# Performance work log

Measured on AMD Instinct MI355X. Metric: run time of the kernel, lower is better.

## Reference

```python
import jax, jax.numpy as jnp
import numpy as np

NUM_HEADS = 8
NUM_GROUPS = 32
EPS = 1e-5


def setup_inputs() -> dict:
    key = jax.random.key(0)
    k1, k2, k3 = jax.random.split(key, 3)
    B, C, H, W = 2, 512, 64, 64
    x = jax.random.normal(k1, (B, C, H, W), dtype=jnp.float32)
    gn_weight = jnp.ones((C,), dtype=jnp.float32)
    gn_bias = jnp.zeros((C,), dtype=jnp.float32)
    # small init so softmax logits are well-conditioned
    w_qkv = jax.random.normal(k2, (3 * C, C), dtype=jnp.float32) * 0.02
    w_proj = jax.random.normal(k3, (C, C), dtype=jnp.float32) * 0.02
    b_proj = jnp.zeros((C,), dtype=jnp.float32)
    return {"x": x, "gn_weight": gn_weight, "gn_bias": gn_bias,
            "w_qkv": w_qkv, "w_proj": w_proj, "b_proj": b_proj}


def group_norm(x, weight, bias):
    B, C, H, W = x.shape
    xg = x.reshape(B, NUM_GROUPS, C // NUM_GROUPS, H, W)
    mean = xg.mean(axis=(2, 3, 4), keepdims=True)
    var = xg.var(axis=(2, 3, 4), keepdims=True)
    xg = (xg - mean) * jax.lax.rsqrt(var + EPS)
    x = xg.reshape(B, C, H, W)
    return x * weight[None, :, None, None] + bias[None, :, None, None]


def reference(x, gn_weight, gn_bias, w_qkv, w_proj, b_proj):
    B, C, H, W = x.shape
    nh = NUM_HEADS
    hd = C // nh
    N = H * W

    h = group_norm(x, gn_weight, gn_bias)
    # 1x1 conv == per-pixel matmul: [B,3C,H,W]
    qkv = jnp.einsum('bchw,oc->bohw', h, w_qkv)
    # (B,3,nh,hd,N) -> (3,B,nh,N,hd)
    qkv = qkv.reshape(B, 3, nh, hd, N).transpose(1, 0, 2, 4, 3)
    q, k, v = qkv[0], qkv[1], qkv[2]

    scale = hd ** -0.5
    attn = jax.nn.softmax(jnp.einsum('bhnd,bhmd->bhnm', q, k) * scale, axis=-1)
    out = jnp.einsum('bhnm,bhmd->bhnd', attn, v)  # [B,nh,N,hd]
    out = out.transpose(0, 1, 3, 2).reshape(B, C, H, W)
    out = jnp.einsum('bchw,oc->bohw', out, w_proj) + b_proj[None, :, None, None]
    return x + out
```

## Files before the change

kernel.cpp:

```cpp
#include <hip/hip_runtime.h>
#include <math.h>

#define BB 2
#define CC 512
#define NN 4096
#define NH 8
#define HD 64
#define NG 32
#define CPG 16

typedef __attribute__((ext_vector_type(8))) short short8;
typedef __attribute__((ext_vector_type(4))) float f32x4;
typedef __attribute__((ext_vector_type(16))) float f32x16;
typedef __attribute__((ext_vector_type(2))) unsigned int u32x2;

typedef __attribute__((address_space(1))) void glb_t;
typedef __attribute__((address_space(3))) void lds_t;

__device__ __forceinline__ void async16(const void* g, void* l) {
  __builtin_amdgcn_global_load_lds((const glb_t*)g, (lds_t*)l, 16, 0, 0);
}

__device__ __forceinline__ unsigned short f2bf(float f) {
  unsigned int u = __float_as_uint(f);
  u += 0x7fffu + ((u >> 16) & 1u);
  return (unsigned short)(u >> 16);
}

__device__ __forceinline__ unsigned int cvt_pk_bf16(float a, float b) {
  unsigned int r;
  asm("v_cvt_pk_bf16_f32 %0, %1, %2" : "=v"(r) : "v"(a), "v"(b));
  return r;
}

__global__ __launch_bounds__(256) void k_gnstats(const float* __restrict__ x,
                                                 float* __restrict__ stats) {
  int b = blockIdx.x >> 5, g = blockIdx.x & 31;
  const float4* p = (const float4*)(x + (size_t)(b * CC + g * CPG) * NN);
  double s = 0.0, sq = 0.0;
  for (int i = threadIdx.x; i < (CPG * NN) / 4; i += 256) {
    float4 v = p[i];
    s  += (double)v.x + (double)v.y + (double)v.z + (double)v.w;
    sq += (double)v.x * v.x + (double)v.y * v.y + (double)v.z * v.z + (double)v.w * v.w;
  }
  __shared__ double red[512];
  red[threadIdx.x] = s; red[256 + threadIdx.x] = sq;
  __syncthreads();
  for (int off = 128; off > 0; off >>= 1) {
    if (threadIdx.x < off) {
      red[threadIdx.x] += red[threadIdx.x + off];
      red[256 + threadIdx.x] += red[256 + threadIdx.x + off];
    }
    __syncthreads();
  }
  if (threadIdx.x == 0) {
    double mean = red[0] / (double)(CPG * NN);
    double var  = red[256] / (double)(CPG * NN) - mean * mean;
    stats[(b * NG + g) * 2]     = (float)mean;
    stats[(b * NG + g) * 2 + 1] = (float)(1.0 / sqrt(var + 1e-5));
  }
}

__global__ __launch_bounds__(256) void k_gnapply(const float* __restrict__ x,
                                                 const float* __restrict__ gw,
                                                 const float* __restrict__ gb,
                                                 const float* __restrict__ stats,
                                                 unsigned short* __restrict__ hT) {
  int bid = blockIdx.x;
  int b = bid >> 9;
  int c0 = ((bid >> 6) & 7) * 64;
  int n0 = (bid & 63) * 64;
  __shared__ float tile[64 * 65];
  int t = threadIdx.x;
#pragma unroll
  for (int i = 0; i < 16; ++i) {
    int e = i * 256 + t, c = e >> 6, n = e & 63;
    int cg = c0 + c, g = cg >> 4;
    float mu = stats[(b * NG + g) * 2], rs = stats[(b * NG + g) * 2 + 1];
    float v = x[(size_t)(b * CC + cg) * NN + n0 + n];
    tile[c * 65 + n] = (v - mu) * rs * gw[cg] + gb[cg];
  }
  __syncthreads();
#pragma unroll
  for (int i = 0; i < 16; ++i) {
    int e = i * 256 + t, n = e >> 6, c = e & 63;
    hT[(size_t)(b * NN + n0 + n) * CC + c0 + c] = f2bf(tile[c * 65 + n]);
  }
}

__global__ __launch_bounds__(256) void k_cvt(const float* __restrict__ src,
                                             unsigned short* __restrict__ dst) {
  int i = (blockIdx.x * 256 + threadIdx.x) * 4;
  float4 v = *(const float4*)(src + i);
  ushort4 o;
  o.x = f2bf(v.x); o.y = f2bf(v.y); o.z = f2bf(v.z); o.w = f2bf(v.w);
  *(ushort4*)(dst + i) = o;
}

__device__ __forceinline__ void gemm_mainloop(const unsigned short* __restrict__ A,
                                              const unsigned short* __restrict__ Bm,
                                              char* smem, int m0, int n0,
                                              f32x4 acc[4][4]) {
  const int t = threadIdx.x, wave = t >> 6, lane = t & 63;
  const int l15 = lane & 15, lhi = lane >> 4;
  const int wr = wave >> 1, wc = wave & 1;
  const f32x4 fz = {0.f, 0.f, 0.f, 0.f};
#pragma unroll
  for (int mi = 0; mi < 4; ++mi)
#pragma unroll
    for (int ni = 0; ni < 4; ++ni) acc[mi][ni] = fz;

  for (int kt = 0; kt < 8; ++kt) {
    __syncthreads();
#pragma unroll
    for (int issue = 0; issue < 4; ++issue) {
      int slot = issue * 256 + t;
      int row = slot >> 3, g = slot & 7;
      async16(A + (size_t)(m0 + row) * 512 + kt * 64 + g * 8,
              smem + issue * 4096 + wave * 1024);
      async16(Bm + (size_t)(n0 + row) * 512 + kt * 64 + g * 8,
              smem + 16384 + issue * 4096 + wave * 1024);
    }
    __syncthreads();
#pragma unroll
    for (int kk = 0; kk < 2; ++kk) {
      short8 a[4], bf[4];
#pragma unroll
      for (int mi = 0; mi < 4; ++mi)
        a[mi] = *(const short8*)(smem + (wr * 64 + mi * 16 + l15) * 128 + kk * 64 + lhi * 16);
#pragma unroll
      for (int ni = 0; ni < 4; ++ni)
        bf[ni] = *(const short8*)(smem + 16384 + (wc * 64 + ni * 16 + l15) * 128 + kk * 64 + lhi * 16);
#pragma unroll
      for (int mi = 0; mi < 4; ++mi)
#pragma unroll
        for (int ni = 0; ni < 4; ++ni)
          acc[mi][ni] = __builtin_amdgcn_mfma_f32_16x16x32_bf16(a[mi], bf[ni], acc[mi][ni], 0, 0, 0);
    }
  }
}

__global__ __launch_bounds__(256) void k_qkvgemm(const unsigned short* __restrict__ hT,
                                                 const unsigned short* __restrict__ Wq,
                                                 unsigned short* __restrict__ Qp,
                                                 unsigned short* __restrict__ Kp,
                                                 unsigned short* __restrict__ vRM) {
  __shared__ char smem[32768];
  f32x4 acc[4][4];
  int m0 = blockIdx.x * 128, n0 = blockIdx.y * 128;
  gemm_mainloop(hT, Wq, smem, m0, n0, acc);
  const int t = threadIdx.x, wave = t >> 6, lane = t & 63;
  const int l15 = lane & 15, lhi = lane >> 4;
  const int wr = wave >> 1, wc = wave & 1;
#pragma unroll
  for (int mi = 0; mi < 4; ++mi)
#pragma unroll
    for (int ni = 0; ni < 4; ++ni)
#pragma unroll
      for (int r = 0; r < 4; ++r) {
        int m = m0 + wr * 64 + mi * 16 + lhi * 4 + r;
        int o = n0 + wc * 64 + ni * 16 + l15;
        unsigned short bf = f2bf(acc[mi][ni][r]);
        int bb = m >> 12, n = m & 4095;
        int h = (o >> 6) & 7, c = o & 63;
        int bh = bb * 8 + h;
        if (o >= 1024) {
          vRM[((size_t)bh * 4096 + n) * 64 + c] = bf;
        } else {
          int tt2 = n >> 6, blk = (n >> 5) & 1, l31 = n & 31;
          int kk = c >> 4, lh2 = (c >> 3) & 1, oct = c & 7;
          unsigned short* base = (o < 512) ? Qp : Kp;
          base[((((size_t)bh * 64 + tt2) * 8 + blk * 4 + kk) << 9) + lh2 * 256 + l31 * 8 + oct] = bf;
        }
      }
}

__global__ __launch_bounds__(256) void k_vtransP(const unsigned short* __restrict__ vRM,
                                                 unsigned short* __restrict__ Vp) {
  int bid = blockIdx.x;
  int bh = bid >> 6, tt = bid & 63;
  __shared__ unsigned short tile[64 * 72];
  int t = threadIdx.x;
  {
    int row = t >> 2, c0 = (t & 3) * 16;
    const short8* src = (const short8*)(vRM + ((size_t)bh * 4096 + tt * 64 + row) * 64 + c0);
    short8 a0 = src[0], a1 = src[1];
    *(short8*)(tile + row * 72 + c0) = a0;
    *(short8*)(tile + row * 72 + c0 + 8) = a1;
  }
  __syncthreads();
#pragma unroll
  for (int ss = 0; ss < 2; ++ss) {
    int s = ss * 256 + t;
    int p = s >> 6, l = s & 63;
    int d = (p & 1) * 32 + (l & 31);
    int kl = (p >> 2) * 32 + ((p >> 1) & 1) * 16 + (l >> 5) * 8;
    short8 v;
#pragma unroll
    for (int j = 0; j < 8; ++j) v[j] = (short)tile[(kl + j) * 72 + d];
    *(short8*)(Vp + (((size_t)(bh * 64 + tt) * 8 + p) << 9) + l * 8) = v;
  }
}

__global__ __launch_bounds__(256) void k_attn(const unsigned short* __restrict__ Qp,
                                              const unsigned short* __restrict__ Kp,
                                              const unsigned short* __restrict__ Vp,
                                              unsigned short* __restrict__ att) {
  __shared__ char smem[32768];
  const int t = threadIdx.x, wave = t >> 6, lane = t & 63;
  const int l31 = lane & 31, lh = lane >> 5;
  const int wq = wave >> 1, wk = wave & 1;
  int bid0 = blockIdx.x;
  int bid = (bid0 & 7) * 128 + (bid0 >> 3);
  int bh = bid >> 6, qt = bid & 63;
  int b = bh >> 3, h = bh & 7;
  const float C = 0.125f * 1.4426950408889634f;

  const char* kCur = (const char*)Kp + (size_t)bh * 524288;
  const char* vCur = (const char*)Vp + (size_t)bh * 524288;
  const char* qSrc = (const char*)Qp + (size_t)bh * 524288 + (size_t)qt * 8192;

#pragma unroll
  for (int i = 0; i < 2; ++i) {
    int p = i * 4 + wave;
    async16(qSrc + p * 1024 + lane * 16, smem + 16384 + p * 1024);
    async16(kCur + p * 1024 + lane * 16, smem + p * 1024);
    async16(vCur + p * 1024 + lane * 16, smem + 8192 + p * 1024);
  }
  kCur += 8192; vCur += 8192;

  const int rbK = wk * 4096 + lane * 16;
  const int rbV = 8192 + wk * 4096 + lane * 16;
  const int rbQ = 16384 + wq * 4096 + lane * 16;

  __syncthreads();
  short8 qa[4];
#pragma unroll
  for (int kk = 0; kk < 4; ++kk)
    qa[kk] = *(const short8*)(smem + rbQ + kk * 1024);
  __syncthreads();

  f32x16 o0 = (f32x16)0.f, o1 = (f32x16)0.f;
  float lsum = 0.f;

#define ATTN_BODY(CURB, NXTB)                                                          \
  {                                                                                    \
    _Pragma("unroll")                                                                  \
    for (int i = 0; i < 2; ++i) {                                                      \
      int p = i * 4 + wave;                                                            \
      async16(kCur + p * 1024 + lane * 16, smem + (NXTB) + p * 1024);                  \
      async16(vCur + p * 1024 + lane * 16, smem + (NXTB) + 8192 + p * 1024);           \
    }                                                                                  \
    kCur += 8192; vCur += 8192;                                                        \
    f32x16 sT = (f32x16)0.f;                                                           \
    __builtin_amdgcn_s_setprio(1);                                                     \
    _Pragma("unroll")                                                                  \
    for (int kk = 0; kk < 4; ++kk) {                                                   \
      short8 ka = *(const short8*)(smem + (CURB) + rbK + kk * 1024);                   \
      sT = __builtin_amdgcn_mfma_f32_32x32x16_bf16(ka, qa[kk], sT, 0, 0, 0);           \
    }                                                                                  \
    __builtin_amdgcn_s_setprio(0);                                                     \
    float ls0 = 0.f, ls1 = 0.f;                                                        \
    _Pragma("unroll")                                                                  \
    for (int r = 0; r < 16; r += 2) {                                                  \
      sT[r]     = __builtin_amdgcn_exp2f(sT[r] * C);                                   \
      sT[r + 1] = __builtin_amdgcn_exp2f(sT[r + 1] * C);                               \
      ls0 += sT[r]; ls1 += sT[r + 1];                                                  \
    }                                                                                  \
    lsum += ls0 + ls1;                                                                 \
    __builtin_amdgcn_s_setprio(1);                                                     \
    _Pragma("unroll")                                                                  \
    for (int kc = 0; kc < 2; ++kc) {                                                   \
      int rb = kc * 8;                                                                 \
      unsigned int x0 = cvt_pk_bf16(sT[rb],     sT[rb + 1]);                           \
      unsigned int x1 = cvt_pk_bf16(sT[rb + 2], sT[rb + 3]);                           \
      unsigned int x2 = cvt_pk_bf16(sT[rb + 4], sT[rb + 5]);                           \
      unsigned int x3 = cvt_pk_bf16(sT[rb + 6], sT[rb + 7]);                           \
      unsigned int u0 = x0, u1 = x1, u2 = x2, u3 = x3;                                 \
      asm("v_permlane32_swap_b32 %0, %1" : "+v"(x0), "+v"(u0));                        \
      asm("v_permlane32_swap_b32 %0, %1" : "+v"(x1), "+v"(u1));                        \
      asm("v_permlane32_swap_b32 %0, %1" : "+v"(x2), "+v"(u2));                        \
      asm("v_permlane32_swap_b32 %0, %1" : "+v"(x3), "+v"(u3));                        \
      union { unsigned int d[4]; short8 s; } pb;                                       \
      pb.d[0] = lh ? x2 : x0;                                                          \
      pb.d[1] = lh ? x3 : x1;                                                          \
      pb.d[2] = lh ? u2 : u0;                                                          \
      pb.d[3] = lh ? u3 : u1;                                                          \
      short8 va0 = *(const short8*)(smem + (CURB) + rbV + kc * 2048);                  \
      o0 = __builtin_amdgcn_mfma_f32_32x32x16_bf16(va0, pb.s, o0, 0, 0, 0);            \
      short8 va1 = *(const short8*)(smem + (CURB) + rbV + kc * 2048 + 1024);           \
      o1 = __builtin_amdgcn_mfma_f32_32x32x16_bf16(va1, pb.s, o1, 0, 0, 0);            \
    }                                                                                  \
    __builtin_amdgcn_s_setprio(0);                                                     \
    __syncthreads();                                                                   \
  }

  for (int it2 = 0; it2 < 32; ++it2) {
    ATTN_BODY(0, 16384)
    ATTN_BODY(16384, 0)
  }
#undef ATTN_BODY

  lsum += __shfl_xor(lsum, 32, 64);
  if (wk) {
    char* os = smem + wq * 8192;
#pragma unroll
    for (int dt = 0; dt < 2; ++dt)
#pragma unroll
      for (int rp = 0; rp < 4; ++rp) {
        f32x4 v;
        v[0] = (dt ? o1 : o0)[4 * rp];     v[1] = (dt ? o1 : o0)[4 * rp + 1];
        v[2] = (dt ? o1 : o0)[4 * rp + 2]; v[3] = (dt ? o1 : o0)[4 * rp + 3];
        *(f32x4*)(os + (dt * 4 + rp) * 1024 + lane * 16) = v;
      }
    *(float*)(smem + 16384 + wq * 256 + lane * 4) = lsum;
  }
  __syncthreads();
  if (!wk) {
    float lt = lsum + *(const float*)(smem + 16384 + wq * 256 + lane * 4);
    float rl = 1.f / lt;
    const char* os = smem + wq * 8192;
#pragma unroll
    for (int dt = 0; dt < 2; ++dt)
#pragma unroll
      for (int rp = 0; rp < 4; ++rp) {
        f32x4 v = *(const f32x4*)(os + (dt * 4 + rp) * 1024 + lane * 16);
        if (dt) {
          o1[4 * rp] += v[0]; o1[4 * rp + 1] += v[1];
          o1[4 * rp + 2] += v[2]; o1[4 * rp + 3] += v[3];
        } else {
          o0[4 * rp] += v[0]; o0[4 * rp + 1] += v[1];
          o0[4 * rp + 2] += v[2]; o0[4 * rp + 3] += v[3];
        }
      }
    unsigned short* abase = att + (size_t)(b * NN + qt * 64 + wq * 32 + l31) * CC + h * 64 + 4 * lh;
#pragma unroll
    for (int dt = 0; dt < 2; ++dt)
#pragma unroll
      for (int rp = 0; rp < 8; ++rp) {
        float e0 = (dt ? o1 : o0)[2 * rp], e1 = (dt ? o1 : o0)[2 * rp + 1];
        unsigned int w = cvt_pk_bf16(e0 * rl, e1 * rl);
        *(unsigned int*)(abase + 32 * dt + 8 * (rp >> 1) + 2 * (rp & 1)) = w;
      }
  }
}

__global__ __launch_bounds__(256) void k_projgemm(const unsigned short* __restrict__ att,
                                                  const unsigned short* __restrict__ Wp,
                                                  const float* __restrict__ x,
                                                  const float* __restrict__ bproj,
                                                  float* __restrict__ out) {
  __shared__ char smem[33280];
  f32x4 acc[4][4];
  int m0 = blockIdx.x * 128, n0 = blockIdx.y * 128;
  gemm_mainloop(att, Wp, smem, m0, n0, acc);
  const int t = threadIdx.x, wave = t >> 6, lane = t & 63;
  const int l15 = lane & 15, lhi = lane >> 4;
  const int wr = wave >> 1, wc = wave & 1;
  __syncthreads();
  float* stg = (float*)(smem + wave * 8320);
  int b = m0 >> 12;
  int nbase = (m0 & 4095) + wr * 64;
#pragma unroll
  for (int half = 0; half < 2; ++half) {
#pragma unroll
    for (int nl = 0; nl < 2; ++nl) {
      int ni = half * 2 + nl;
#pragma unroll
      for (int mi = 0; mi < 4; ++mi)
#pragma unroll
        for (int r = 0; r < 4; ++r) {
          int cl = nl * 16 + l15;
          int row = mi * 16 + lhi * 4 + r;
          stg[cl * 65 + row] = acc[mi][ni][r];
        }
    }
#pragma unroll 4
    for (int i = 0; i < 32; ++i) {
      int oc = n0 + wc * 64 + half * 32 + i;
      float v = stg[i * 65 + lane];
      size_t idx = (size_t)(b * CC + oc) * NN + nbase + lane;
      out[idx] = x[idx] + v + bproj[oc];
    }
    __syncthreads();
  }
}

extern "C" void kernel_launch(void* const* d_in, const int* in_sizes, int n_in,
                              void* d_out, int out_size, void* d_ws, size_t ws_size,
                              hipStream_t stream) {
  const float* x     = (const float*)d_in[0];
  const float* gw    = (const float*)d_in[1];
  const float* gb    = (const float*)d_in[2];
  const float* wqkv  = (const float*)d_in[3];
  const float* wproj = (const float*)d_in[4];
  const float* bproj = (const float*)d_in[5];
  float* out = (float*)d_out;
  char* ws = (char*)d_ws;

  unsigned short* Qp     = (unsigned short*)(ws + 0);
  unsigned short* Kp     = (unsigned short*)(ws + 8388608);
  unsigned short* vRM    = (unsigned short*)(ws + 16777216);
  unsigned short* attb   = (unsigned short*)(ws + 16777216);
  unsigned short* hTb    = (unsigned short*)(ws + 25165824);
  unsigned short* Vp     = (unsigned short*)(ws + 25165824);
  unsigned short* wqkvb  = (unsigned short*)(ws + 33554432);
  unsigned short* wprojb = (unsigned short*)(ws + 35127296);
  float*          stats  = (float*)(ws + 35651584);

  k_gnstats<<<64, 256, 0, stream>>>(x, stats);
  k_gnapply<<<1024, 256, 0, stream>>>(x, gw, gb, stats, hTb);
  k_cvt<<<768, 256, 0, stream>>>(wqkv, wqkvb);
  k_cvt<<<256, 256, 0, stream>>>(wproj, wprojb);
  k_qkvgemm<<<dim3(64, 12), 256, 0, stream>>>(hTb, wqkvb, Qp, Kp, vRM);
  k_vtransP<<<1024, 256, 0, stream>>>(vRM, Vp);
  k_attn<<<1024, 256, 0, stream>>>(Qp, Kp, Vp, attb);
  k_projgemm<<<dim3(64, 4), 256, 0, stream>>>(attb, wprojb, x, bproj, out);
}
```

Before: 261.2 us.

## Fuse preprocessing kernels, write packed V from QKV GEMM, fold softmax scale into Q

Merges the GroupNorm stats and the two weight-conversion launches into one kernel. The QKV GEMM epilogue now stages its tile in LDS and writes Q, K and V in packed MFMA layout with coalesced 16-byte stores, which removes the separate V transpose kernel and the vRM buffer. The softmax scale and log2e are folded into Q, and the P-fragment repacking in attention drops the select ops by using permlane swaps directly. The GroupNorm apply kernel is vectorised to float4 loads and short8 stores. Risks: Q is rounded to bf16 after scaling, and the reworked index maps and permlane pairing must match the attention kernel's expected layout.

```diff
diff --git a/kernel.cpp b/kernel.cpp
--- a/kernel.cpp
+++ b/kernel.cpp
@@ -12,7 +12,6 @@
 typedef __attribute__((ext_vector_type(8))) short short8;
 typedef __attribute__((ext_vector_type(4))) float f32x4;
 typedef __attribute__((ext_vector_type(16))) float f32x16;
-typedef __attribute__((ext_vector_type(2))) unsigned int u32x2;
 
 typedef __attribute__((address_space(1))) void glb_t;
 typedef __attribute__((address_space(3))) void lds_t;
@@ -33,9 +32,22 @@
   return r;
 }
 
-__global__ __launch_bounds__(256) void k_gnstats(const float* __restrict__ x,
-                                                 float* __restrict__ stats) {
-  int b = blockIdx.x >> 5, g = blockIdx.x & 31;
+__global__ __launch_bounds__(256) void k_pre(const float* __restrict__ x,
+                                             const float* __restrict__ wqkv,
+                                             const float* __restrict__ wproj,
+                                             float* __restrict__ stats,
+                                             unsigned short* __restrict__ wb) {
+  int bid = blockIdx.x;
+  if (bid >= 64) {
+    int i = ((bid - 64) * 256 + threadIdx.x) * 4;
+    const float* src = (i < 786432) ? (wqkv + i) : (wproj + (i - 786432));
+    float4 v = *(const float4*)src;
+    ushort4 o;
+    o.x = f2bf(v.x); o.y = f2bf(v.y); o.z = f2bf(v.z); o.w = f2bf(v.w);
+    *(ushort4*)(wb + i) = o;
+    return;
+  }
+  int b = bid >> 5, g = bid & 31;
   const float4* p = (const float4*)(x + (size_t)(b * CC + g * CPG) * NN);
   double s = 0.0, sq = 0.0;
   for (int i = threadIdx.x; i < (CPG * NN) / 4; i += 256) {
@@ -70,31 +82,32 @@
   int b = bid >> 9;
   int c0 = ((bid >> 6) & 7) * 64;
   int n0 = (bid & 63) * 64;
-  __shared__ float tile[64 * 65];
+  __shared__ float tile[64 * 68];
   int t = threadIdx.x;
 #pragma unroll
-  for (int i = 0; i < 16; ++i) {
-    int e = i * 256 + t, c = e >> 6, n = e & 63;
+  for (int i = 0; i < 4; ++i) {
+    int idx = i * 256 + t;
+    int c = idx >> 4, n4 = (idx & 15) * 4;
     int cg = c0 + c, g = cg >> 4;
     float mu = stats[(b * NG + g) * 2], rs = stats[(b * NG + g) * 2 + 1];
-    float v = x[(size_t)(b * CC + cg) * NN + n0 + n];
-    tile[c * 65 + n] = (v - mu) * rs * gw[cg] + gb[cg];
-  }
-  __syncthreads();
-#pragma unroll
-  for (int i = 0; i < 16; ++i) {
-    int e = i * 256 + t, n = e >> 6, c = e & 63;
-    hT[(size_t)(b * NN + n0 + n) * CC + c0 + c] = f2bf(tile[c * 65 + n]);
-  }
-}
-
-__global__ __launch_bounds__(256) void k_cvt(const float* __restrict__ src,
-                                             unsigned short* __restrict__ dst) {
-  int i = (blockIdx.x * 256 + threadIdx.x) * 4;
-  float4 v = *(const float4*)(src + i);
-  ushort4 o;
-  o.x = f2bf(v.x); o.y = f2bf(v.y); o.z = f2bf(v.z); o.w = f2bf(v.w);
-  *(ushort4*)(dst + i) = o;
+    float w = gw[cg], bb = gb[cg];
+    float4 v = *(const float4*)(x + (size_t)(b * CC + cg) * NN + n0 + n4);
+    float* dst = tile + c * 68 + n4;
+    dst[0] = (v.x - mu) * rs * w + bb;
+    dst[1] = (v.y - mu) * rs * w + bb;
+    dst[2] = (v.z - mu) * rs * w + bb;
+    dst[3] = (v.w - mu) * rs * w + bb;
+  }
+  __syncthreads();
+#pragma unroll
+  for (int i = 0; i < 2; ++i) {
+    int idx = i * 256 + t;
+    int n = idx >> 3, c8 = (idx & 7) * 8;
+    short8 o;
+#pragma unroll
+    for (int j = 0; j < 8; ++j) o[j] = (short)f2bf(tile[(c8 + j) * 68 + n]);
+    *(short8*)(hT + (size_t)(b * NN + n0 + n) * CC + c0 + c8) = o;
+  }
 }
 
 __device__ __forceinline__ void gemm_mainloop(const unsigned short* __restrict__ A,
@@ -144,7 +157,7 @@
                                                  const unsigned short* __restrict__ Wq,
                                                  unsigned short* __restrict__ Qp,
                                                  unsigned short* __restrict__ Kp,
-                                                 unsigned short* __restrict__ vRM) {
+                                                 unsigned short* __restrict__ Vp) {
   __shared__ char smem[32768];
   f32x4 acc[4][4];
   int m0 = blockIdx.x * 128, n0 = blockIdx.y * 128;
@@ -152,53 +165,43 @@
   const int t = threadIdx.x, wave = t >> 6, lane = t & 63;
   const int l15 = lane & 15, lhi = lane >> 4;
   const int wr = wave >> 1, wc = wave & 1;
+  const int type = n0 >> 9;
+  const int h0 = (n0 >> 6) & 7;
+  __syncthreads();
+  unsigned short* lim = (unsigned short*)smem;
+  const float qs = 0.18033688011112042f;
 #pragma unroll
   for (int mi = 0; mi < 4; ++mi)
 #pragma unroll
     for (int ni = 0; ni < 4; ++ni)
 #pragma unroll
       for (int r = 0; r < 4; ++r) {
-        int m = m0 + wr * 64 + mi * 16 + lhi * 4 + r;
-        int o = n0 + wc * 64 + ni * 16 + l15;
-        unsigned short bf = f2bf(acc[mi][ni][r]);
-        int bb = m >> 12, n = m & 4095;
-        int h = (o >> 6) & 7, c = o & 63;
-        int bh = bb * 8 + h;
-        if (o >= 1024) {
-          vRM[((size_t)bh * 4096 + n) * 64 + c] = bf;
-        } else {
-          int tt2 = n >> 6, blk = (n >> 5) & 1, l31 = n & 31;
-          int kk = c >> 4, lh2 = (c >> 3) & 1, oct = c & 7;
-          unsigned short* base = (o < 512) ? Qp : Kp;
-          base[((((size_t)bh * 64 + tt2) * 8 + blk * 4 + kk) << 9) + lh2 * 256 + l31 * 8 + oct] = bf;
-        }
+        int pr = wr * 64 + mi * 16 + lhi * 4 + r;
+        int oc = wc * 64 + ni * 16 + l15;
+        int hh = oc >> 6, c = oc & 63;
+        int tt2 = pr >> 6, pn = pr & 63;
+        int idx;
+        if (type < 2)
+          idx = ((hh * 2 + tt2) * 8 + ((pn >> 5) << 2) + (c >> 4)) * 512
+              + ((c >> 3) & 1) * 256 + (pn & 31) * 8 + (c & 7);
+        else
+          idx = ((hh * 2 + tt2) * 8 + ((pn >> 5) << 2) + (((pn >> 4) & 1) << 1) + (c >> 5)) * 512
+              + ((pn >> 3) & 1) * 256 + (c & 31) * 8 + (pn & 7);
+        float v = acc[mi][ni][r];
+        if (type == 0) v *= qs;
+        lim[idx] = f2bf(v);
       }
-}
-
-__global__ __launch_bounds__(256) void k_vtransP(const unsigned short* __restrict__ vRM,
-                                                 unsigned short* __restrict__ Vp) {
-  int bid = blockIdx.x;
-  int bh = bid >> 6, tt = bid & 63;
-  __shared__ unsigned short tile[64 * 72];
-  int t = threadIdx.x;
-  {
-    int row = t >> 2, c0 = (t & 3) * 16;
-    const short8* src = (const short8*)(vRM + ((size_t)bh * 4096 + tt * 64 + row) * 64 + c0);
-    short8 a0 = src[0], a1 = src[1];
-    *(short8*)(tile + row * 72 + c0) = a0;
-    *(short8*)(tile + row * 72 + c0 + 8) = a1;
-  }
-  __syncthreads();
-#pragma unroll
-  for (int ss = 0; ss < 2; ++ss) {
-    int s = ss * 256 + t;
-    int p = s >> 6, l = s & 63;
-    int d = (p & 1) * 32 + (l & 31);
-    int kl = (p >> 2) * 32 + ((p >> 1) & 1) * 16 + (l >> 5) * 8;
-    short8 v;
-#pragma unroll
-    for (int j = 0; j < 8; ++j) v[j] = (short)tile[(kl + j) * 72 + d];
-    *(short8*)(Vp + (((size_t)(bh * 64 + tt) * 8 + p) << 9) + l * 8) = v;
+  __syncthreads();
+  unsigned short* gbp = type == 0 ? Qp : (type == 1 ? Kp : Vp);
+  int b = m0 >> 12, tile0 = (m0 & 4095) >> 6;
+#pragma unroll
+  for (int i = 0; i < 8; ++i) {
+    int cidx = i * 256 + t;
+    int pg = cidx >> 6;
+    int bh = b * 8 + h0 + (pg >> 4);
+    size_t dst = (size_t)bh * 262144 + (size_t)(tile0 + ((pg >> 3) & 1)) * 4096
+               + (size_t)(pg & 7) * 512 + (size_t)(cidx & 63) * 8;
+    *(short8*)(gbp + dst) = *(const short8*)(lim + cidx * 8);
   }
 }
 
@@ -214,7 +217,6 @@
   int bid = (bid0 & 7) * 128 + (bid0 >> 3);
   int bh = bid >> 6, qt = bid & 63;
   int b = bh >> 3, h = bh & 7;
-  const float C = 0.125f * 1.4426950408889634f;
 
   const char* kCur = (const char*)Kp + (size_t)bh * 524288;
   const char* vCur = (const char*)Vp + (size_t)bh * 524288;
@@ -263,8 +265,8 @@
     float ls0 = 0.f, ls1 = 0.f;                                                        \
     _Pragma("unroll")                                                                  \
     for (int r = 0; r < 16; r += 2) {                                                  \
-      sT[r]     = __builtin_amdgcn_exp2f(sT[r] * C);                                   \
-      sT[r + 1] = __builtin_amdgcn_exp2f(sT[r + 1] * C);                               \
+      sT[r]     = __builtin_amdgcn_exp2f(sT[r]);                                       \
+      sT[r + 1] = __builtin_amdgcn_exp2f(sT[r + 1]);                                   \
       ls0 += sT[r]; ls1 += sT[r + 1];                                                  \
     }                                                                                  \
     lsum += ls0 + ls1;                                                                 \
@@ -276,16 +278,10 @@
       unsigned int x1 = cvt_pk_bf16(sT[rb + 2], sT[rb + 3]);                           \
       unsigned int x2 = cvt_pk_bf16(sT[rb + 4], sT[rb + 5]);                           \
       unsigned int x3 = cvt_pk_bf16(sT[rb + 6], sT[rb + 7]);                           \
-      unsigned int u0 = x0, u1 = x1, u2 = x2, u3 = x3;                                 \
-      asm("v_permlane32_swap_b32 %0, %1" : "+v"(x0), "+v"(u0));                        \
-      asm("v_permlane32_swap_b32 %0, %1" : "+v"(x1), "+v"(u1));                        \
-      asm("v_permlane32_swap_b32 %0, %1" : "+v"(x2), "+v"(u2));                        \
-      asm("v_permlane32_swap_b32 %0, %1" : "+v"(x3), "+v"(u3));                        \
+      asm("v_permlane32_swap_b32 %0, %1" : "+v"(x0), "+v"(x2));                        \
+      asm("v_permlane32_swap_b32 %0, %1" : "+v"(x1), "+v"(x3));                        \
       union { unsigned int d[4]; short8 s; } pb;                                       \
-      pb.d[0] = lh ? x2 : x0;                                                          \
-      pb.d[1] = lh ? x3 : x1;                                                          \
-      pb.d[2] = lh ? u2 : u0;                                                          \
-      pb.d[3] = lh ? u3 : u1;                                                          \
+      pb.d[0] = x0; pb.d[1] = x1; pb.d[2] = x2; pb.d[3] = x3;                          \
       short8 va0 = *(const short8*)(smem + (CURB) + rbV + kc * 2048);                  \
       o0 = __builtin_amdgcn_mfma_f32_32x32x16_bf16(va0, pb.s, o0, 0, 0, 0);            \
       short8 va1 = *(const short8*)(smem + (CURB) + rbV + kc * 2048 + 1024);           \
@@ -400,20 +396,16 @@
 
   unsigned short* Qp     = (unsigned short*)(ws + 0);
   unsigned short* Kp     = (unsigned short*)(ws + 8388608);
-  unsigned short* vRM    = (unsigned short*)(ws + 16777216);
-  unsigned short* attb   = (unsigned short*)(ws + 16777216);
+  unsigned short* Vp     = (unsigned short*)(ws + 16777216);
   unsigned short* hTb    = (unsigned short*)(ws + 25165824);
-  unsigned short* Vp     = (unsigned short*)(ws + 25165824);
+  unsigned short* attb   = (unsigned short*)(ws + 25165824);
   unsigned short* wqkvb  = (unsigned short*)(ws + 33554432);
   unsigned short* wprojb = (unsigned short*)(ws + 35127296);
   float*          stats  = (float*)(ws + 35651584);
 
-  k_gnstats<<<64, 256, 0, stream>>>(x, stats);
+  k_pre<<<1088, 256, 0, stream>>>(x, wqkv, wproj, stats, wqkvb);
   k_gnapply<<<1024, 256, 0, stream>>>(x, gw, gb, stats, hTb);
-  k_cvt<<<768, 256, 0, stream>>>(wqkv, wqkvb);
-  k_cvt<<<256, 256, 0, stream>>>(wproj, wprojb);
-  k_qkvgemm<<<dim3(64, 12), 256, 0, stream>>>(hTb, wqkvb, Qp, Kp, vRM);
-  k_vtransP<<<1024, 256, 0, stream>>>(vRM, Vp);
+  k_qkvgemm<<<dim3(64, 12), 256, 0, stream>>>(hTb, wqkvb, Qp, Kp, Vp);
   k_attn<<<1024, 256, 0, stream>>>(Qp, Kp, Vp, attb);
   k_projgemm<<<dim3(64, 4), 256, 0, stream>>>(attb, wprojb, x, bproj, out);
 }
```

Measured after the change: 235.8 us. 1.11x faster.
